# Performance work log

Hardware: AMD Instinct MI355X
Metric: run time of the kernel (lower is better)

Reference implementation:

```python
import jax, jax.numpy as jnp
import numpy as np

N = 10000
E = 160000
DIMS = [256, 256, 256, 256]
EPS = 1e-5
DSCALE = 1.0
SPE_IDX = 0


def setup_inputs() -> dict:
    key = jax.random.key(0)
    ks = jax.random.split(key, 40)
    inp = {}
    inp['x'] = jax.random.normal(ks[0], (N, DIMS[0]), dtype=jnp.float32)
    inp['src'] = jax.random.randint(ks[1], (E,), 0, N, dtype=jnp.int32)
    inp['dst'] = jax.random.randint(ks[2], (E,), 0, N, dtype=jnp.int32)
    k = 3
    for i, (din, dout) in enumerate(zip(DIMS[:-1], DIMS[1:])):
        s = 1.0 / np.sqrt(din)
        inp[f'Ws{i}'] = jax.random.uniform(ks[k], (din, dout), jnp.float32, -s, s); k += 1
        inp[f'Wn{i}'] = jax.random.uniform(ks[k], (din, dout), jnp.float32, -s, s); k += 1
        inp[f'b{i}'] = jnp.zeros((dout,), jnp.float32)
        inp[f'g{i}'] = jnp.ones((dout,), jnp.float32)
        inp[f'be{i}'] = jnp.zeros((dout,), jnp.float32)
    return inp


def _sage(h, src, dst, Ws, Wn, b):
    # mean aggregation over in-neighbors: segment-sum gathered src feats over dst
    agg = jax.ops.segment_sum(h[src], dst, num_segments=N)          # [N, din]
    deg = jax.ops.segment_sum(jnp.ones((E,), h.dtype), dst, num_segments=N)
    mean = agg / jnp.maximum(deg, 1.0)[:, None]
    return h @ Ws + mean @ Wn + b


def _bn(h, g, be):
    # BatchNorm1d, training mode (biased batch variance)
    mu = jnp.mean(h, axis=0)
    var = jnp.mean((h - mu) ** 2, axis=0)
    return (h - mu) * jax.lax.rsqrt(var + EPS) * g + be


def reference(x, src, dst, Ws0, Wn0, b0, g0, be0, Ws1, Wn1, b1, g1, be1,
              Ws2, Wn2, b2, g2, be2):
    params = [(Ws0, Wn0, b0, g0, be0), (Ws1, Wn1, b1, g1, be1),
              (Ws2, Wn2, b2, g2, be2)]
    n_layers = len(params)
    outs = x
    for i, (Ws, Wn, b, g, be) in enumerate(params):
        outs = _sage(outs, src, dst, Ws, Wn, b)
        # hid side-outputs (sigmoid(outs*dscale)[spe_idx]) don't affect outs path
        outs = _bn(outs, g, be)
        if i != n_layers - 1:
            outs = jax.nn.relu(outs)
        else:
            outs = jax.nn.sigmoid(outs)
    return outs
```

## Files before the change

kernel.cpp:

```cpp
#include <hip/hip_runtime.h>
#include <math.h>

#define NN 10000
#define EE 160000
#define DIM 256
#define KK 512
#define CAP 128
#define EPS_BN 1e-5f
#define NTILES 626

typedef __attribute__((ext_vector_type(8)))  short bf16x8;
typedef __attribute__((ext_vector_type(16))) float f32x16;

static __device__ __forceinline__ unsigned short f2bf(float f) {
    unsigned u = __float_as_uint(f);
    unsigned r = (u + 0x7fffu + ((u >> 16) & 1u)) >> 16;
    return (unsigned short)r;
}
static __device__ __forceinline__ float bflo(unsigned v) { return __uint_as_float(v << 16); }
static __device__ __forceinline__ float bfhi(unsigned v) { return __uint_as_float(v & 0xffff0000u); }
static __device__ __forceinline__ unsigned packbf(float a, float b) {
    return (unsigned)f2bf(a) | ((unsigned)f2bf(b) << 16);
}

struct Params {
    const float* x; const int* src; const int* dst;
    const float *Ws0, *Wn0, *Ws1, *Wn1, *Ws2, *Wn2;
    const float *g0, *be0, *g1, *be1, *g2, *be2;
    float* out;
    unsigned short* hcat;
    unsigned short* zbuf;
    unsigned short* wcat;
    float* stats;
    int* cnt;
    int* slots;
};

static __device__ __forceinline__ void accum8(float* a, uint4 v) {
    a[0] += bflo(v.x); a[1] += bfhi(v.x);
    a[2] += bflo(v.y); a[3] += bfhi(v.y);
    a[4] += bflo(v.z); a[5] += bfhi(v.z);
    a[6] += bflo(v.w); a[7] += bfhi(v.w);
}
static __device__ __forceinline__ void accum8n(float* a, uint4 v,
                                               const float* sc, const float* sh) {
    a[0] += fmaxf(bflo(v.x) * sc[0] + sh[0], 0.f);
    a[1] += fmaxf(bfhi(v.x) * sc[1] + sh[1], 0.f);
    a[2] += fmaxf(bflo(v.y) * sc[2] + sh[2], 0.f);
    a[3] += fmaxf(bfhi(v.y) * sc[3] + sh[3], 0.f);
    a[4] += fmaxf(bflo(v.z) * sc[4] + sh[4], 0.f);
    a[5] += fmaxf(bfhi(v.z) * sc[5] + sh[5], 0.f);
    a[6] += fmaxf(bflo(v.w) * sc[6] + sh[6], 0.f);
    a[7] += fmaxf(bfhi(v.w) * sc[7] + sh[7], 0.f);
}

__global__ __launch_bounds__(256) void k_prep(Params P) {
    int g0 = blockIdx.x * 256 + threadIdx.x;
    int stride = gridDim.x * 256;
    for (int g = g0; g < NN * 64; g += stride) {
        int r = g >> 6, c4 = (g & 63) * 4;
        float4 v = *(const float4*)(P.x + (size_t)r * DIM + c4);
        uint2 p; p.x = packbf(v.x, v.y); p.y = packbf(v.z, v.w);
        *(uint2*)(P.hcat + (size_t)r * KK + c4) = p;
    }
    for (int g = g0; g < 3 * DIM * KK; g += stride) {
        int L = g >> 17; int i = g & 131071;
        int k = i >> 8, n = i & 255;
        const float* Ws = (L == 0) ? P.Ws0 : ((L == 1) ? P.Ws1 : P.Ws2);
        const float* Wn = (L == 0) ? P.Wn0 : ((L == 1) ? P.Wn1 : P.Wn2);
        float v = (k < DIM) ? Ws[(size_t)k * DIM + n] : Wn[(size_t)(k - DIM) * DIM + n];
        P.wcat[(size_t)L * DIM * KK + (size_t)n * KK + k] = f2bf(v);
    }
    for (int g = g0; g < NN + 6 * DIM; g += stride) {
        if (g < NN) P.cnt[g] = 0;
        else P.stats[g - NN] = 0.f;
    }
}

__global__ __launch_bounds__(256) void k_bucket(Params P) {
    int e = blockIdx.x * 256 + threadIdx.x;
    if (e < EE) {
        int d = P.dst[e];
        int p = atomicAdd(&P.cnt[d], 1);
        if (p < CAP) P.slots[(size_t)d * CAP + p] = P.src[e];
    }
}

__global__ __launch_bounds__(256) void k_agg(Params P, int L) {
    int t = threadIdx.x;
    int wave = t >> 6, lane = t & 63;
    int h = lane >> 5, l = lane & 31;
    float sc[8], sh[8];
    if (L > 0) {
        const float* st = P.stats + (L - 1) * 2 * DIM;
        const float* gam = (L == 1) ? P.g0 : P.g1;
        const float* bet = (L == 1) ? P.be0 : P.be1;
#pragma unroll
        for (int i = 0; i < 8; ++i) {
            int c = l * 8 + i;
            float mu  = st[c] * (1.0f / NN);
            float var = st[DIM + c] * (1.0f / NN) - mu * mu;
            float k = rsqrtf(var + EPS_BN) * gam[c];
            sc[i] = k;
            sh[i] = bet[c] - mu * k;
        }
    }
    const uint4* zsrc = (const uint4*)P.zbuf;
    const uint4* hsrc = (const uint4*)P.hcat;
    uint4* hdst = (uint4*)P.hcat;

    int node = blockIdx.x * 4 + wave;
    int cnt = P.cnt[node]; if (cnt > CAP) cnt = CAP;
    const int* sl = P.slots + (size_t)node * CAP;
    float a[8] = {0, 0, 0, 0, 0, 0, 0, 0};

    if (L > 0 && h == 0) {
        uint4 z = zsrc[(size_t)node * 32 + l];
        uint4 p;
        p.x = packbf(fmaxf(bflo(z.x) * sc[0] + sh[0], 0.f),
                     fmaxf(bfhi(z.x) * sc[1] + sh[1], 0.f));
        p.y = packbf(fmaxf(bflo(z.y) * sc[2] + sh[2], 0.f),
                     fmaxf(bfhi(z.y) * sc[3] + sh[3], 0.f));
        p.z = packbf(fmaxf(bflo(z.z) * sc[4] + sh[4], 0.f),
                     fmaxf(bfhi(z.z) * sc[5] + sh[5], 0.f));
        p.w = packbf(fmaxf(bflo(z.w) * sc[6] + sh[6], 0.f),
                     fmaxf(bfhi(z.w) * sc[7] + sh[7], 0.f));
        hdst[(size_t)node * 64 + l] = p;
    }

    int j = h;
    if (L == 0) {
        for (; j + 6 < cnt; j += 8) {
            int i0 = sl[j],     i1 = sl[j + 2];
            int i2 = sl[j + 4], i3 = sl[j + 6];
            uint4 v0 = hsrc[(size_t)i0 * 64 + l];
            uint4 v1 = hsrc[(size_t)i1 * 64 + l];
            uint4 v2 = hsrc[(size_t)i2 * 64 + l];
            uint4 v3 = hsrc[(size_t)i3 * 64 + l];
            accum8(a, v0); accum8(a, v1); accum8(a, v2); accum8(a, v3);
        }
        for (; j < cnt; j += 2) accum8(a, hsrc[(size_t)sl[j] * 64 + l]);
    } else {
        for (; j + 6 < cnt; j += 8) {
            int i0 = sl[j],     i1 = sl[j + 2];
            int i2 = sl[j + 4], i3 = sl[j + 6];
            uint4 v0 = zsrc[(size_t)i0 * 32 + l];
            uint4 v1 = zsrc[(size_t)i1 * 32 + l];
            uint4 v2 = zsrc[(size_t)i2 * 32 + l];
            uint4 v3 = zsrc[(size_t)i3 * 32 + l];
            accum8n(a, v0, sc, sh); accum8n(a, v1, sc, sh);
            accum8n(a, v2, sc, sh); accum8n(a, v3, sc, sh);
        }
        for (; j < cnt; j += 2) accum8n(a, zsrc[(size_t)sl[j] * 32 + l], sc, sh);
    }
#pragma unroll
    for (int q = 0; q < 8; ++q) a[q] += __shfl_xor(a[q], 32);
    if (h == 0) {
        float inv = 1.0f / (float)(cnt > 1 ? cnt : 1);
        uint4 p;
        p.x = packbf(a[0] * inv, a[1] * inv);
        p.y = packbf(a[2] * inv, a[3] * inv);
        p.z = packbf(a[4] * inv, a[5] * inv);
        p.w = packbf(a[6] * inv, a[7] * inv);
        hdst[(size_t)node * 64 + 32 + l] = p;
    }
}

__global__ __launch_bounds__(256) void k_gemm(Params P, int L) {
    const unsigned short* wcatL = P.wcat + (size_t)L * DIM * KK;
    float* statsL = P.stats + L * 2 * DIM;
    int t = threadIdx.x;
    int wave = t >> 6, lane = t & 63;
    int m = lane & 31, half = lane >> 5;
    int tile = blockIdx.x;
    int rowt = tile >> 1, colh = tile & 1;
    int row0 = rowt * 32;
    int colw0 = colh * 128 + wave * 32;
    int ar = row0 + m; if (ar > NN - 1) ar = NN - 1;
    const unsigned short* Ap = P.hcat + (size_t)ar * KK + half * 8;
    const unsigned short* Bp = wcatL + (size_t)(colw0 + m) * KK + half * 8;
    f32x16 acc;
#pragma unroll
    for (int i = 0; i < 16; ++i) acc[i] = 0.f;
#pragma unroll 8
    for (int k0 = 0; k0 < KK; k0 += 16) {
        bf16x8 av = *(const bf16x8*)(Ap + k0);
        bf16x8 bv = *(const bf16x8*)(Bp + k0);
        acc = __builtin_amdgcn_mfma_f32_32x32x16_bf16(av, bv, acc, 0, 0, 0);
    }
    int cc = colw0 + m;
    float s = 0.f, s2 = 0.f;
#pragma unroll
    for (int reg = 0; reg < 16; ++reg) {
        int r = row0 + (reg & 3) + 8 * (reg >> 2) + 4 * half;
        if (r < NN) {
            float v = acc[reg];
            P.zbuf[(size_t)r * DIM + cc] = f2bf(v);
            s += v; s2 += v * v;
        }
    }
    s  += __shfl_down(s, 32);
    s2 += __shfl_down(s2, 32);
    if (half == 0) {
        atomicAdd(&statsL[cc], s);
        atomicAdd(&statsL[DIM + cc], s2);
    }
}

__global__ __launch_bounds__(256) void k_norm(Params P) {
    const float* statsL = P.stats + 2 * 2 * DIM;
    int t = threadIdx.x;
    int c8 = (t & 31) * 8;
    int r = blockIdx.x * 8 + (t >> 5);
    float sc[8], sh[8];
#pragma unroll
    for (int i = 0; i < 8; ++i) {
        int c = c8 + i;
        float mu  = statsL[c] * (1.0f / NN);
        float var = statsL[DIM + c] * (1.0f / NN) - mu * mu;
        float k = rsqrtf(var + EPS_BN) * P.g2[c];
        sc[i] = k;
        sh[i] = P.be2[c] - mu * k;
    }
    uint4 v = *(const uint4*)(P.zbuf + (size_t)r * DIM + c8);
    float f[8] = {bflo(v.x), bfhi(v.x), bflo(v.y), bfhi(v.y),
                  bflo(v.z), bfhi(v.z), bflo(v.w), bfhi(v.w)};
#pragma unroll
    for (int i = 0; i < 8; ++i) f[i] = f[i] * sc[i] + sh[i];
    float4 o0, o1;
    o0.x = 1.0f / (1.0f + __expf(-f[0]));
    o0.y = 1.0f / (1.0f + __expf(-f[1]));
    o0.z = 1.0f / (1.0f + __expf(-f[2]));
    o0.w = 1.0f / (1.0f + __expf(-f[3]));
    o1.x = 1.0f / (1.0f + __expf(-f[4]));
    o1.y = 1.0f / (1.0f + __expf(-f[5]));
    o1.z = 1.0f / (1.0f + __expf(-f[6]));
    o1.w = 1.0f / (1.0f + __expf(-f[7]));
    *(float4*)(P.out + (size_t)r * DIM + c8)     = o0;
    *(float4*)(P.out + (size_t)r * DIM + c8 + 4) = o1;
}

extern "C" void kernel_launch(void* const* d_in, const int* in_sizes, int n_in,
                              void* d_out, int out_size, void* d_ws, size_t ws_size,
                              hipStream_t stream) {
    Params P;
    P.x   = (const float*)d_in[0];
    P.src = (const int*)d_in[1];
    P.dst = (const int*)d_in[2];
    P.Ws0 = (const float*)d_in[3];  P.Wn0 = (const float*)d_in[4];
    P.g0  = (const float*)d_in[6];  P.be0 = (const float*)d_in[7];
    P.Ws1 = (const float*)d_in[8];  P.Wn1 = (const float*)d_in[9];
    P.g1  = (const float*)d_in[11]; P.be1 = (const float*)d_in[12];
    P.Ws2 = (const float*)d_in[13]; P.Wn2 = (const float*)d_in[14];
    P.g2  = (const float*)d_in[16]; P.be2 = (const float*)d_in[17];
    P.out = (float*)d_out;

    char* ws = (char*)d_ws;
    size_t off = 0;
    P.hcat = (unsigned short*)(ws + off); off += (size_t)NN * KK * 2;
    P.zbuf = (unsigned short*)(ws + off); off += (size_t)NN * DIM * 2;
    P.wcat = (unsigned short*)(ws + off); off += (size_t)3 * DIM * KK * 2;
    P.stats = (float*)(ws + off); off += 3 * 2 * DIM * sizeof(float);
    P.cnt   = (int*)(ws + off); off += (size_t)NN * 4; off = (off + 255) & ~(size_t)255;
    P.slots = (int*)(ws + off); off += (size_t)NN * CAP * 4;
    (void)ws_size;

    k_prep<<<1024, 256, 0, stream>>>(P);
    k_bucket<<<(EE + 255) / 256, 256, 0, stream>>>(P);
    for (int L = 0; L < 3; ++L) {
        k_agg<<<NN / 4, 256, 0, stream>>>(P, L);
        k_gemm<<<NTILES, 256, 0, stream>>>(P, L);
    }
    k_norm<<<NN / 8, 256, 0, stream>>>(P);
}
```

Baseline: 241.6 us.

## Fuse neighbor aggregation into GEMM via shared-memory A tile per block

Merges the aggregation and GEMM kernels into one kernel. Each 512-thread block gathers 32 nodes' self and mean-neighbor features into an LDS tile, then runs MFMA against the concatenated weights for all 256 output columns. This removes the global round trip of the concatenated hcat buffer and three kernel launches, and ping-pongs z buffers between layers. The cost is that grid parallelism drops to 313 blocks, and the gather phase uses only 4 nodes per wave serially, which may lower occupancy and latency hiding.

After: 224.2 us. 1.08x faster.

```diff
diff --git a/kernel.cpp b/kernel.cpp
--- a/kernel.cpp
+++ b/kernel.cpp
@@ -7,10 +7,12 @@
 #define KK 512
 #define CAP 128
 #define EPS_BN 1e-5f
-#define NTILES 626
+#define AST 516
 
 typedef __attribute__((ext_vector_type(8)))  short bf16x8;
 typedef __attribute__((ext_vector_type(16))) float f32x16;
+
+union U16 { uint2 u2[2]; bf16x8 v; };
 
 static __device__ __forceinline__ unsigned short f2bf(float f) {
     unsigned u = __float_as_uint(f);
@@ -28,8 +30,9 @@
     const float *Ws0, *Wn0, *Ws1, *Wn1, *Ws2, *Wn2;
     const float *g0, *be0, *g1, *be1, *g2, *be2;
     float* out;
-    unsigned short* hcat;
-    unsigned short* zbuf;
+    unsigned short* hx;
+    unsigned short* z0;
+    unsigned short* z1;
     unsigned short* wcat;
     float* stats;
     int* cnt;
@@ -61,7 +64,7 @@
         int r = g >> 6, c4 = (g & 63) * 4;
         float4 v = *(const float4*)(P.x + (size_t)r * DIM + c4);
         uint2 p; p.x = packbf(v.x, v.y); p.y = packbf(v.z, v.w);
-        *(uint2*)(P.hcat + (size_t)r * KK + c4) = p;
+        *(uint2*)(P.hx + (size_t)r * DIM + c4) = p;
     }
     for (int g = g0; g < 3 * DIM * KK; g += stride) {
         int L = g >> 17; int i = g & 131071;
@@ -86,10 +89,14 @@
     }
 }
 
-__global__ __launch_bounds__(256) void k_agg(Params P, int L) {
+__global__ __launch_bounds__(512) void k_ag(Params P, int L,
+                                            const unsigned short* __restrict__ gsrc,
+                                            unsigned short* __restrict__ gdst) {
+    __shared__ unsigned short At[32][AST];
     int t = threadIdx.x;
     int wave = t >> 6, lane = t & 63;
     int h = lane >> 5, l = lane & 31;
+
     float sc[8], sh[8];
     if (L > 0) {
         const float* st = P.stats + (L - 1) * 2 * DIM;
@@ -105,86 +112,94 @@
             sh[i] = bet[c] - mu * k;
         }
     }
-    const uint4* zsrc = (const uint4*)P.zbuf;
-    const uint4* hsrc = (const uint4*)P.hcat;
-    uint4* hdst = (uint4*)P.hcat;
-
-    int node = blockIdx.x * 4 + wave;
-    int cnt = P.cnt[node]; if (cnt > CAP) cnt = CAP;
-    const int* sl = P.slots + (size_t)node * CAP;
-    float a[8] = {0, 0, 0, 0, 0, 0, 0, 0};
-
-    if (L > 0 && h == 0) {
-        uint4 z = zsrc[(size_t)node * 32 + l];
-        uint4 p;
-        p.x = packbf(fmaxf(bflo(z.x) * sc[0] + sh[0], 0.f),
-                     fmaxf(bfhi(z.x) * sc[1] + sh[1], 0.f));
-        p.y = packbf(fmaxf(bflo(z.y) * sc[2] + sh[2], 0.f),
-                     fmaxf(bfhi(z.y) * sc[3] + sh[3], 0.f));
-        p.z = packbf(fmaxf(bflo(z.z) * sc[4] + sh[4], 0.f),
-                     fmaxf(bfhi(z.z) * sc[5] + sh[5], 0.f));
-        p.w = packbf(fmaxf(bflo(z.w) * sc[6] + sh[6], 0.f),
-                     fmaxf(bfhi(z.w) * sc[7] + sh[7], 0.f));
-        hdst[(size_t)node * 64 + l] = p;
-    }
-
-    int j = h;
-    if (L == 0) {
-        for (; j + 6 < cnt; j += 8) {
-            int i0 = sl[j],     i1 = sl[j + 2];
-            int i2 = sl[j + 4], i3 = sl[j + 6];
-            uint4 v0 = hsrc[(size_t)i0 * 64 + l];
-            uint4 v1 = hsrc[(size_t)i1 * 64 + l];
-            uint4 v2 = hsrc[(size_t)i2 * 64 + l];
-            uint4 v3 = hsrc[(size_t)i3 * 64 + l];
-            accum8(a, v0); accum8(a, v1); accum8(a, v2); accum8(a, v3);
-        }
-        for (; j < cnt; j += 2) accum8(a, hsrc[(size_t)sl[j] * 64 + l]);
-    } else {
-        for (; j + 6 < cnt; j += 8) {
-            int i0 = sl[j],     i1 = sl[j + 2];
-            int i2 = sl[j + 4], i3 = sl[j + 6];
-            uint4 v0 = zsrc[(size_t)i0 * 32 + l];
-            uint4 v1 = zsrc[(size_t)i1 * 32 + l];
-            uint4 v2 = zsrc[(size_t)i2 * 32 + l];
-            uint4 v3 = zsrc[(size_t)i3 * 32 + l];
-            accum8n(a, v0, sc, sh); accum8n(a, v1, sc, sh);
-            accum8n(a, v2, sc, sh); accum8n(a, v3, sc, sh);
-        }
-        for (; j < cnt; j += 2) accum8n(a, zsrc[(size_t)sl[j] * 32 + l], sc, sh);
-    }
-#pragma unroll
-    for (int q = 0; q < 8; ++q) a[q] += __shfl_xor(a[q], 32);
-    if (h == 0) {
-        float inv = 1.0f / (float)(cnt > 1 ? cnt : 1);
-        uint4 p;
-        p.x = packbf(a[0] * inv, a[1] * inv);
-        p.y = packbf(a[2] * inv, a[3] * inv);
-        p.z = packbf(a[4] * inv, a[5] * inv);
-        p.w = packbf(a[6] * inv, a[7] * inv);
-        hdst[(size_t)node * 64 + 32 + l] = p;
-    }
-}
-
-__global__ __launch_bounds__(256) void k_gemm(Params P, int L) {
+    const uint4* srcm = (const uint4*)gsrc;
+
+    for (int i = 0; i < 4; ++i) {
+        int m = wave * 4 + i;
+        int node = blockIdx.x * 32 + m;
+        unsigned short* arow = &At[m][0];
+        if (node >= NN) {
+            if (h == 0) {
+                uint2 z2 = make_uint2(0u, 0u);
+                *(uint2*)(arow + l * 8)           = z2;
+                *(uint2*)(arow + l * 8 + 4)       = z2;
+                *(uint2*)(arow + 256 + l * 8)     = z2;
+                *(uint2*)(arow + 256 + l * 8 + 4) = z2;
+            }
+            continue;
+        }
+        int cnt = P.cnt[node]; if (cnt > CAP) cnt = CAP;
+        const int* sl = P.slots + (size_t)node * CAP;
+        if (h == 0) {
+            uint4 z = srcm[(size_t)node * 32 + l];
+            uint4 o;
+            if (L > 0) {
+                o.x = packbf(fmaxf(bflo(z.x) * sc[0] + sh[0], 0.f),
+                             fmaxf(bfhi(z.x) * sc[1] + sh[1], 0.f));
+                o.y = packbf(fmaxf(bflo(z.y) * sc[2] + sh[2], 0.f),
+                             fmaxf(bfhi(z.y) * sc[3] + sh[3], 0.f));
+                o.z = packbf(fmaxf(bflo(z.z) * sc[4] + sh[4], 0.f),
+                             fmaxf(bfhi(z.z) * sc[5] + sh[5], 0.f));
+                o.w = packbf(fmaxf(bflo(z.w) * sc[6] + sh[6], 0.f),
+                             fmaxf(bfhi(z.w) * sc[7] + sh[7], 0.f));
+            } else o = z;
+            *(uint2*)(arow + l * 8)     = make_uint2(o.x, o.y);
+            *(uint2*)(arow + l * 8 + 4) = make_uint2(o.z, o.w);
+        }
+        float a[8] = {0, 0, 0, 0, 0, 0, 0, 0};
+        int j = h;
+        if (L == 0) {
+            for (; j + 6 < cnt; j += 8) {
+                int i0 = sl[j],     i1 = sl[j + 2];
+                int i2 = sl[j + 4], i3 = sl[j + 6];
+                uint4 v0 = srcm[(size_t)i0 * 32 + l];
+                uint4 v1 = srcm[(size_t)i1 * 32 + l];
+                uint4 v2 = srcm[(size_t)i2 * 32 + l];
+                uint4 v3 = srcm[(size_t)i3 * 32 + l];
+                accum8(a, v0); accum8(a, v1); accum8(a, v2); accum8(a, v3);
+            }
+            for (; j < cnt; j += 2) accum8(a, srcm[(size_t)sl[j] * 32 + l]);
+        } else {
+            for (; j + 6 < cnt; j += 8) {
+                int i0 = sl[j],     i1 = sl[j + 2];
+                int i2 = sl[j + 4], i3 = sl[j + 6];
+                uint4 v0 = srcm[(size_t)i0 * 32 + l];
+                uint4 v1 = srcm[(size_t)i1 * 32 + l];
+                uint4 v2 = srcm[(size_t)i2 * 32 + l];
+                uint4 v3 = srcm[(size_t)i3 * 32 + l];
+                accum8n(a, v0, sc, sh); accum8n(a, v1, sc, sh);
+                accum8n(a, v2, sc, sh); accum8n(a, v3, sc, sh);
+            }
+            for (; j < cnt; j += 2) accum8n(a, srcm[(size_t)sl[j] * 32 + l], sc, sh);
+        }
+#pragma unroll
+        for (int q = 0; q < 8; ++q) a[q] += __shfl_xor(a[q], 32);
+        if (h == 0) {
+            float inv = 1.0f / (float)(cnt > 1 ? cnt : 1);
+            *(uint2*)(arow + 256 + l * 8)     = make_uint2(packbf(a[0] * inv, a[1] * inv),
+                                                           packbf(a[2] * inv, a[3] * inv));
+            *(uint2*)(arow + 256 + l * 8 + 4) = make_uint2(packbf(a[4] * inv, a[5] * inv),
+                                                           packbf(a[6] * inv, a[7] * inv));
+        }
+    }
+    __syncthreads();
+
     const unsigned short* wcatL = P.wcat + (size_t)L * DIM * KK;
     float* statsL = P.stats + L * 2 * DIM;
-    int t = threadIdx.x;
-    int wave = t >> 6, lane = t & 63;
-    int m = lane & 31, half = lane >> 5;
-    int tile = blockIdx.x;
-    int rowt = tile >> 1, colh = tile & 1;
-    int row0 = rowt * 32;
-    int colw0 = colh * 128 + wave * 32;
-    int ar = row0 + m; if (ar > NN - 1) ar = NN - 1;
-    const unsigned short* Ap = P.hcat + (size_t)ar * KK + half * 8;
-    const unsigned short* Bp = wcatL + (size_t)(colw0 + m) * KK + half * 8;
+    int m = l;
+    int row0 = blockIdx.x * 32;
+    int colw0 = wave * 32;
+    const unsigned short* Bp = wcatL + (size_t)(colw0 + m) * KK + h * 8;
+    const unsigned short* Arow = &At[m][0];
     f32x16 acc;
 #pragma unroll
     for (int i = 0; i < 16; ++i) acc[i] = 0.f;
 #pragma unroll 8
     for (int k0 = 0; k0 < KK; k0 += 16) {
-        bf16x8 av = *(const bf16x8*)(Ap + k0);
+        U16 ua;
+        ua.u2[0] = *(const uint2*)(Arow + k0 + h * 8);
+        ua.u2[1] = *(const uint2*)(Arow + k0 + h * 8 + 4);
+        bf16x8 av = ua.v;
         bf16x8 bv = *(const bf16x8*)(Bp + k0);
         acc = __builtin_amdgcn_mfma_f32_32x32x16_bf16(av, bv, acc, 0, 0, 0);
     }
@@ -192,16 +207,16 @@
     float s = 0.f, s2 = 0.f;
 #pragma unroll
     for (int reg = 0; reg < 16; ++reg) {
-        int r = row0 + (reg & 3) + 8 * (reg >> 2) + 4 * half;
+        int r = row0 + (reg & 3) + 8 * (reg >> 2) + 4 * h;
         if (r < NN) {
             float v = acc[reg];
-            P.zbuf[(size_t)r * DIM + cc] = f2bf(v);
+            gdst[(size_t)r * DIM + cc] = f2bf(v);
             s += v; s2 += v * v;
         }
     }
     s  += __shfl_down(s, 32);
     s2 += __shfl_down(s2, 32);
-    if (half == 0) {
+    if (h == 0) {
         atomicAdd(&statsL[cc], s);
         atomicAdd(&statsL[DIM + cc], s2);
     }
@@ -222,7 +237,7 @@
         sc[i] = k;
         sh[i] = P.be2[c] - mu * k;
     }
-    uint4 v = *(const uint4*)(P.zbuf + (size_t)r * DIM + c8);
+    uint4 v = *(const uint4*)(P.z0 + (size_t)r * DIM + c8);
     float f[8] = {bflo(v.x), bfhi(v.x), bflo(v.y), bfhi(v.y),
                   bflo(v.z), bfhi(v.z), bflo(v.w), bfhi(v.w)};
 #pragma unroll
@@ -257,19 +272,19 @@
 
     char* ws = (char*)d_ws;
     size_t off = 0;
-    P.hcat = (unsigned short*)(ws + off); off += (size_t)NN * KK * 2;
-    P.zbuf = (unsigned short*)(ws + off); off += (size_t)NN * DIM * 2;
+    P.hx   = (unsigned short*)(ws + off); off += (size_t)NN * DIM * 2;
+    P.z0   = (unsigned short*)(ws + off); off += (size_t)NN * DIM * 2;
+    P.z1   = (unsigned short*)(ws + off); off += (size_t)NN * DIM * 2;
     P.wcat = (unsigned short*)(ws + off); off += (size_t)3 * DIM * KK * 2;
     P.stats = (float*)(ws + off); off += 3 * 2 * DIM * sizeof(float);
     P.cnt   = (int*)(ws + off); off += (size_t)NN * 4; off = (off + 255) & ~(size_t)255;
     P.slots = (int*)(ws + off); off += (size_t)NN * CAP * 4;
     (void)ws_size;
 
-    k_prep<<<1024, 256, 0, stream>>>(P);
+    k_prep<<<512, 256, 0, stream>>>(P);
     k_bucket<<<(EE + 255) / 256, 256, 0, stream>>>(P);
-    for (int L = 0; L < 3; ++L) {
-        k_agg<<<NN / 4, 256, 0, stream>>>(P, L);
-        k_gemm<<<NTILES, 256, 0, stream>>>(P, L);
-    }
+    k_ag<<<313, 512, 0, stream>>>(P, 0, P.hx, P.z0);
+    k_ag<<<313, 512, 0, stream>>>(P, 1, P.z0, P.z1);
+    k_ag<<<313, 512, 0, stream>>>(P, 2, P.z1, P.z0);
     k_norm<<<NN / 8, 256, 0, stream>>>(P);
 }
```
